# Performance work log

Hardware: AMD Instinct MI355X
Metric: run time of the kernel (lower is better)

The kernel has to match this reference:

```python
import jax, jax.numpy as jnp
import numpy as np

# Sizes: N nodes, E edges, C channels (atoms/node), CF channel_nf, R relations,
# H hidden/feature dim (uniform across the 2 AM_EGCL layers), L layers.
N, E, C, CF, R, H, L = 10000, 160000, 4, 16, 7, 256, 2
EPS = 1e-5


def setup_inputs() -> dict:
    key = jax.random.key(0)
    ks = jax.random.split(key, 16)
    p = lambda k, shape: (jax.random.normal(k, shape, jnp.float32) * 0.02)
    inp = {
        "input": jax.random.normal(ks[0], (N, H), jnp.float32),
        "coords": jax.random.normal(ks[1], (N, C, 3), jnp.float32),
        "channel_attr": jax.random.normal(ks[2], (N, C, CF), jnp.float32),
        # strictly positive channel weights (atom-occupancy style)
        "channel_weights": jax.random.uniform(ks[3], (N, C), jnp.float32) + 0.5,
        "edge_weights": jax.random.uniform(ks[4], (E,), jnp.float32),
    }
    src = jax.random.randint(ks[5], (E,), 0, N)
    dst = jax.random.randint(ks[6], (E,), 0, N)
    rel = jax.random.randint(ks[7], (E,), 0, R)
    inp["edge_list"] = jnp.stack([src, dst, rel], axis=1)
    ein = 2 * H + CF + 2 * CF  # h_i, h_j, radial feat, pooled channel attr i/j
    inp.update({
        "W_rad": p(ks[8], (L, C * C, CF)), "b_rad": jnp.zeros((L, CF), jnp.float32),
        "W_e1": p(ks[9], (L, ein, H)), "b_e1": jnp.zeros((L, H), jnp.float32),
        "W_e2": p(ks[10], (L, H, H)), "b_e2": jnp.zeros((L, H), jnp.float32),
        "W_c1": p(ks[11], (L, H, H)), "b_c1": jnp.zeros((L, H), jnp.float32),
        "W_c2": p(ks[12], (L, H, C * C)),
        "W_n1": p(ks[13], (L, R * H + H, H)), "b_n1": jnp.zeros((L, H), jnp.float32),
        "W_n2": p(ks[14], (L, H, H)), "b_n2": jnp.zeros((L, H), jnp.float32),
        "ln_g": jnp.ones((L, H), jnp.float32), "ln_b": jnp.zeros((L, H), jnp.float32),
    })
    return inp


def _am_egcl(h, x, edge_list, channel_attr, channel_weights, edge_weights, prm):
    """One adaptive multichannel equivariant graph conv layer."""
    (W_rad, b_rad, W_e1, b_e1, W_e2, b_e2, W_c1, b_c1, W_c2,
     W_n1, b_n1, W_n2, b_n2, ln_g, ln_b) = prm
    row, col, rel = edge_list[:, 0], edge_list[:, 1], edge_list[:, 2]
    # --- multichannel invariant radial features -------------------------------
    xd = x[row][:, :, None, :] - x[col][:, None, :, :]        # [E,C,C,3]
    radial = jnp.sum(xd * xd, axis=-1)                         # [E,C,C]
    wmask = channel_weights[row][:, :, None] * channel_weights[col][:, None, :]
    radial = radial * wmask
    rad_feat = jax.nn.silu(radial.reshape(-1, C * C) @ W_rad + b_rad)  # [E,CF]
    # pooled (weighted-mean) channel attribute per node
    csum = jnp.sum(channel_weights, axis=-1, keepdims=True)
    ca = jnp.sum(channel_attr * channel_weights[..., None], axis=1) / csum  # [N,CF]
    # --- edge message MLP ------------------------------------------------------
    m_in = jnp.concatenate([h[row], h[col], rad_feat, ca[row], ca[col]], axis=-1)
    m = jax.nn.silu(jax.nn.silu(m_in @ W_e1 + b_e1) @ W_e2 + b_e2)  # [E,H]
    m = m * edge_weights[:, None]
    # --- equivariant coord update ---------------------------------------------
    phi = (jax.nn.silu(m @ W_c1 + b_c1) @ W_c2).reshape(-1, C, C)   # [E,C,C]
    trans = jnp.mean(xd * phi[..., None], axis=2)                   # [E,C,3]
    ones = jnp.ones((trans.shape[0],), x.dtype)
    cnt = jnp.maximum(jax.ops.segment_sum(ones, row, num_segments=N), 1.0)
    x_out = x + jax.ops.segment_sum(trans, row, num_segments=N) / cnt[:, None, None]
    # --- relational node aggregation (GearNet-style, per-relation bins) --------
    seg = col * R + rel
    agg = jax.ops.segment_sum(m, seg, num_segments=N * R).reshape(N, R * H)
    h_out = jax.nn.silu(jnp.concatenate([agg, h], axis=-1) @ W_n1 + b_n1) @ W_n2 + b_n2
    # dropout p=0 (eval) -> identity; then LayerNorm
    mu = jnp.mean(h_out, axis=-1, keepdims=True)
    var = jnp.var(h_out, axis=-1, keepdims=True)
    h_out = (h_out - mu) * jax.lax.rsqrt(var + EPS) * ln_g + ln_b
    return h_out, x_out


def reference(input, edge_list, coords, channel_attr, channel_weights, edge_weights,
              W_rad, b_rad, W_e1, b_e1, W_e2, b_e2, W_c1, b_c1, W_c2,
              W_n1, b_n1, W_n2, b_n2, ln_g, ln_b):
    h, x = input, coords
    for i in range(L):  # fixed small layer count
        prm = (W_rad[i], b_rad[i], W_e1[i], b_e1[i], W_e2[i], b_e2[i],
               W_c1[i], b_c1[i], W_c2[i], W_n1[i], b_n1[i], W_n2[i], b_n2[i],
               ln_g[i], ln_b[i])
        h, x = _am_egcl(h, x, edge_list, channel_attr, channel_weights,
                        edge_weights, prm)
    return h, x  # (node_feature [N,H], coord_feature [N,C,3])
```

## Files before the change

### kernel.cpp

```cpp
#include <hip/hip_runtime.h>
#include <hip/hip_bf16.h>

#define NN 10000
#define EE 160000
#define CCH 4
#define CF 16
#define RR 7
#define HH 256
#define NSEG 70000
#define SCB 274
#define EPSV 1e-5f

typedef unsigned short ushort_t;
typedef __bf16 bf16x8 __attribute__((ext_vector_type(8)));
typedef float f32x4 __attribute__((ext_vector_type(4)));

__device__ __forceinline__ float silu_f(float v) {
    float e = __builtin_amdgcn_exp2f(v * -1.442695040888963f);
    return v * __builtin_amdgcn_rcpf(1.f + e);
}

__device__ __forceinline__ ushort_t bf16u(float f) {
    unsigned int u = __builtin_bit_cast(unsigned int, f);
    u += 0x7fffu + ((u >> 16) & 1u);
    return (ushort_t)(u >> 16);
}

__device__ __forceinline__ float ubf2f(ushort_t u) {
    unsigned int v = ((unsigned int)u) << 16;
    return __builtin_bit_cast(float, v);
}


__global__ __launch_bounds__(256) void cab_kernel(
    const float* __restrict__ attr, const float* __restrict__ cw,
    ushort_t* __restrict__ cab16)
{
    int t = blockIdx.x * 256 + threadIdx.x;
    if (t < NN * CF) {
        int n = t >> 4, f = t & 15;
        float s = 0.f, cs = 0.f;
        #pragma unroll
        for (int c = 0; c < CCH; ++c) {
            float w = cw[n * CCH + c];
            s  += attr[(n * CCH + c) * CF + f] * w;
            cs += w;
        }
        cab16[t] = bf16u(s / cs);
    }
}

__global__ __launch_bounds__(256) void cvt_kernel(
    const float* __restrict__ s, ushort_t* __restrict__ d, int n)
{
    int t = blockIdx.x * 256 + threadIdx.x;
    if (t < n) d[t] = bf16u(s[t]);
}

__global__ __launch_bounds__(256) void histdeg_kernel(
    const int* __restrict__ el, int* __restrict__ hist, float* __restrict__ deg)
{
    int e = blockIdx.x * 256 + threadIdx.x;
    if (e < EE) {
        int r = el[e * 3], c = el[e * 3 + 1], rl = el[e * 3 + 2];
        atomicAdd(&hist[c * RR + rl], 1);
        atomicAdd(&deg[r], 1.f);
    }
}

__global__ __launch_bounds__(256) void scan1_kernel(
    const int* __restrict__ hist, int* __restrict__ pscan, int* __restrict__ bsum)
{
    __shared__ int sc[256];
    int b = blockIdx.x, t = threadIdx.x, i = b * 256 + t;
    int v = (i < NSEG) ? hist[i] : 0;
    sc[t] = v; __syncthreads();
    for (int off = 1; off < 256; off <<= 1) {
        int u = (t >= off) ? sc[t - off] : 0;
        __syncthreads();
        sc[t] += u;
        __syncthreads();
    }
    if (i < NSEG) pscan[i] = sc[t] - v;
    if (t == 255) bsum[b] = sc[255];
}

__global__ __launch_bounds__(256) void scan2_kernel(
    const int* __restrict__ bsum, int* __restrict__ bofs, int nb)
{
    __shared__ int sc[512];
    int t = threadIdx.x;
    int o1 = (t < nb) ? bsum[t] : 0;
    int o2 = (t + 256 < nb) ? bsum[t + 256] : 0;
    sc[t] = o1; sc[t + 256] = o2;
    __syncthreads();
    for (int off = 1; off < 512; off <<= 1) {
        int u1 = (t >= off) ? sc[t - off] : 0;
        int u2 = (t + 256 >= off) ? sc[t + 256 - off] : 0;
        __syncthreads();
        sc[t] += u1; sc[t + 256] += u2;
        __syncthreads();
    }
    if (t < nb) bofs[t] = sc[t] - o1;
    if (t + 256 < nb) bofs[t + 256] = sc[t + 256] - o2;
}

__global__ __launch_bounds__(256) void scan3_kernel(
    const int* __restrict__ pscan, const int* __restrict__ bofs, int* __restrict__ segst)
{
    int b = blockIdx.x, t = threadIdx.x, i = b * 256 + t;
    if (i < NSEG) segst[i] = pscan[i] + bofs[b];
    if (i == 0) segst[NSEG] = EE;
}

__global__ __launch_bounds__(256) void scatter_kernel(
    const int* __restrict__ el, const int* __restrict__ segst,
    int* __restrict__ cursor, int* __restrict__ perm)
{
    int e = blockIdx.x * 256 + threadIdx.x;
    if (e < EE) {
        int s = el[e * 3 + 1] * RR + el[e * 3 + 2];
        int pos = segst[s] + atomicAdd(&cursor[s], 1);
        perm[pos] = e;
    }
}


__device__ __forceinline__ void pack_tile(
    const float* __restrict__ W, ushort_t* __restrict__ out,
    int Kreal, int N, int kt, int nt, int NTOT, int lane)
{
    int n = nt * 16 + (lane & 15);
    int kbase = kt * 32 + (lane >> 4) * 8;
    ushort_t* o = out + ((size_t)(kt * NTOT + nt) * 64 + lane) * 8;
    #pragma unroll
    for (int j = 0; j < 8; ++j) {
        int k = kbase + j;
        o[j] = (k < Kreal) ? bf16u(W[(size_t)k * N + n]) : (ushort_t)0;
    }
}

__global__ __launch_bounds__(64) void pack_all_kernel(
    const float* __restrict__ W_e1, const float* __restrict__ W_e2,
    const float* __restrict__ W_c1, const float* __restrict__ W_c2,
    const float* __restrict__ W_n1, const float* __restrict__ W_n2,
    ushort_t* __restrict__ pe1, ushort_t* __restrict__ pe2,
    ushort_t* __restrict__ pc1, ushort_t* __restrict__ pc2,
    ushort_t* __restrict__ pn1, ushort_t* __restrict__ pn2)
{
    int b = blockIdx.x, lane = threadIdx.x;
    int l = 0;
    if (b >= 1704) { l = 1; b -= 1704; }
    if (b < 288) {
        pack_tile(W_e1 + (size_t)l * 143360, pe1 + (size_t)l * 147456,
                  560, 256, b / 16, b & 15, 16, lane);
    } else if (b < 416) {
        int c = b - 288;
        pack_tile(W_e2 + (size_t)l * 65536, pe2 + (size_t)l * 65536,
                  256, 256, c / 16, c & 15, 16, lane);
    } else if (b < 544) {
        int c = b - 416;
        pack_tile(W_c1 + (size_t)l * 65536, pc1 + (size_t)l * 65536,
                  256, 256, c / 16, c & 15, 16, lane);
    } else if (b < 552) {
        int c = b - 544;
        pack_tile(W_c2 + (size_t)l * 4096, pc2 + (size_t)l * 4096,
                  256, 16, c, 0, 1, lane);
    } else if (b < 1576) {
        int c = b - 552;
        pack_tile(W_n1 + (size_t)l * 524288, pn1 + (size_t)l * 524288,
                  2048, 256, c / 16, c & 15, 16, lane);
    } else {
        int c = b - 1576;
        pack_tile(W_n2 + (size_t)l * 65536, pn2 + (size_t)l * 65536,
                  256, 256, c / 16, c & 15, 16, lane);
    }
}


template<int KT, int NTOT>
__device__ __forceinline__ void mfma_stage32(
    const ushort_t (&A)[32][584], int colOff,
    const ushort_t* __restrict__ Wp, int w, int lane,
    f32x4 (&acc)[2][4])
{
    const f32x4 Z = {0.f, 0.f, 0.f, 0.f};
    #pragma unroll
    for (int mt = 0; mt < 2; ++mt)
        #pragma unroll
        for (int j = 0; j < 4; ++j) acc[mt][j] = Z;
    const int ar = lane & 15, aq = (lane >> 4) * 8;
    for (int kt = 0; kt < KT; ++kt) {
        bf16x8 a0 = *(const bf16x8*)&A[ar][colOff + kt * 32 + aq];
        bf16x8 a1 = *(const bf16x8*)&A[16 + ar][colOff + kt * 32 + aq];
        #pragma unroll
        for (int j = 0; j < 4; ++j) {
            bf16x8 b = *(const bf16x8*)(Wp + ((size_t)(kt * NTOT + w * 4 + j) * 64 + lane) * 8);
            acc[0][j] = __builtin_amdgcn_mfma_f32_16x16x32_bf16(a0, b, acc[0][j], 0, 0, 0);
            acc[1][j] = __builtin_amdgcn_mfma_f32_16x16x32_bf16(a1, b, acc[1][j], 0, 0, 0);
        }
    }
}


__global__ __launch_bounds__(256, 4) void edge_kernel(
    const int* __restrict__ el, const int* __restrict__ perm,
    const float* __restrict__ cw,
    const float* __restrict__ ew, const float* __restrict__ x,
    const ushort_t* __restrict__ hb16, const ushort_t* __restrict__ cab16,
    const float* __restrict__ W_rad, const float* __restrict__ b_rad,
    const ushort_t* __restrict__ pe1, const float* __restrict__ b_e1,
    const ushort_t* __restrict__ pe2, const float* __restrict__ b_e2,
    const ushort_t* __restrict__ pc1, const float* __restrict__ b_c1,
    const ushort_t* __restrict__ pc2,
    ushort_t* __restrict__ mb16, float* __restrict__ xacc)
{
    __shared__ ushort_t abuf[32][584];
    __shared__ float radbuf[32][16];
    __shared__ int rowS[32], colS[32];
    __shared__ float ewS[32];

    const int tid = threadIdx.x, lane = tid & 63, w = tid >> 6;
    const int ar = lane & 15, aq = (lane >> 4) * 8, quad = lane >> 4;
    const int e0 = blockIdx.x * 32;

    if (tid < 32) {
        int eg = perm[e0 + tid];
        rowS[tid] = el[eg * 3 + 0];
        colS[tid] = el[eg * 3 + 1];
        ewS[tid]  = ew[eg];
    }
    __syncthreads();

    #pragma unroll
    for (int it = 0; it < 8; ++it) {
        int c = it * 256 + tid;
        int e = c >> 6, half = (c >> 5) & 1, idx = c & 31;
        int node = half ? colS[e] : rowS[e];
        *(uint4*)&abuf[e][half * 256 + idx * 8] =
            ((const uint4*)(hb16 + (size_t)node * 256))[idx];
    }
    if (tid < 128) {
        int e = tid >> 2, half2 = (tid >> 1) & 1, idx = tid & 1;
        int node = half2 ? colS[e] : rowS[e];
        *(uint4*)&abuf[e][528 + half2 * 16 + idx * 8] =
            ((const uint4*)(cab16 + node * 16))[idx];
    } else if (tid < 192) {
        int c = tid - 128, e = c >> 1, idx = c & 1;
        uint4 z = {0u, 0u, 0u, 0u};
        *(uint4*)&abuf[e][560 + idx * 8] = z;
    }
    #pragma unroll
    for (int it = 0; it < 2; ++it) {
        int t = it * 256 + tid;
        int e = t >> 4, ab = t & 15, a = ab >> 2, b = ab & 3;
        int row = rowS[e], col = colS[e];
        float d0 = x[row * 12 + a * 3 + 0] - x[col * 12 + b * 3 + 0];
        float d1 = x[row * 12 + a * 3 + 1] - x[col * 12 + b * 3 + 1];
        float d2 = x[row * 12 + a * 3 + 2] - x[col * 12 + b * 3 + 2];
        radbuf[e][ab] = (d0 * d0 + d1 * d1 + d2 * d2)
                      * cw[row * CCH + a] * cw[col * CCH + b];
    }
    __syncthreads();

    #pragma unroll
    for (int it = 0; it < 2; ++it) {
        int t = it * 256 + tid;
        int e = t >> 4, f = t & 15;
        float acc = b_rad[f];
        #pragma unroll
        for (int ab = 0; ab < 16; ++ab) acc += radbuf[e][ab] * W_rad[ab * 16 + f];
        abuf[e][512 + f] = bf16u(silu_f(acc));
    }
    __syncthreads();

    f32x4 acc[2][4];

    mfma_stage32<18, 16>(abuf, 0, pe1, w, lane, acc);
    __syncthreads();
    #pragma unroll
    for (int j = 0; j < 4; ++j) {
        int n = w * 64 + j * 16 + ar;
        float bj = b_e1[n];
        #pragma unroll
        for (int mt = 0; mt < 2; ++mt)
            #pragma unroll
            for (int r = 0; r < 4; ++r)
                abuf[mt * 16 + quad * 4 + r][288 + n] = bf16u(silu_f(acc[mt][j][r] + bj));
    }
    __syncthreads();

    mfma_stage32<8, 16>(abuf, 288, pe2, w, lane, acc);
    #pragma unroll
    for (int j = 0; j < 4; ++j) {
        int n = w * 64 + j * 16 + ar;
        float bj = b_e2[n];
        #pragma unroll
        for (int mt = 0; mt < 2; ++mt)
            #pragma unroll
            for (int r = 0; r < 4; ++r) {
                int e = mt * 16 + quad * 4 + r;
                abuf[e][n] = bf16u(silu_f(acc[mt][j][r] + bj) * ewS[e]);
            }
    }
    __syncthreads();

    #pragma unroll
    for (int it = 0; it < 4; ++it) {
        int t = it * 256 + tid;
        int e = t >> 5, c = t & 31;
        *(uint4*)(mb16 + ((size_t)(e0 + e) * 256 + c * 8)) =
            *(const uint4*)&abuf[e][c * 8];
    }

    mfma_stage32<8, 16>(abuf, 0, pc1, w, lane, acc);
    #pragma unroll
    for (int j = 0; j < 4; ++j) {
        int n = w * 64 + j * 16 + ar;
        float bj = b_c1[n];
        #pragma unroll
        for (int mt = 0; mt < 2; ++mt)
            #pragma unroll
            for (int r = 0; r < 4; ++r)
                abuf[mt * 16 + quad * 4 + r][288 + n] = bf16u(silu_f(acc[mt][j][r] + bj));
    }
    __syncthreads();

    if (w < 2) {
        const f32x4 Z = {0.f, 0.f, 0.f, 0.f};
        f32x4 p = Z;
        #pragma unroll
        for (int kt = 0; kt < 8; ++kt) {
            bf16x8 a = *(const bf16x8*)&abuf[w * 16 + ar][288 + kt * 32 + aq];
            bf16x8 b = *(const bf16x8*)(pc2 + ((size_t)kt * 64 + lane) * 8);
            p = __builtin_amdgcn_mfma_f32_16x16x32_bf16(a, b, p, 0, 0, 0);
        }
        #pragma unroll
        for (int r = 0; r < 4; ++r)
            radbuf[w * 16 + quad * 4 + r][ar] = p[r];
    }
    __syncthreads();

    for (int t = tid; t < 384; t += 256) {
        int e = t / 12, r = t - e * 12, a = r / 3, k = r - a * 3;
        int row = rowS[e], col = colS[e];
        float xr = x[row * 12 + a * 3 + k];
        float s = 0.f;
        #pragma unroll
        for (int b = 0; b < 4; ++b)
            s += (xr - x[col * 12 + b * 3 + k]) * radbuf[e][a * 4 + b];
        atomicAdd(&xacc[row * 12 + a * 3 + k], 0.25f * s);
    }
}


__global__ __launch_bounds__(256, 3) void node_kernel(
    const ushort_t* __restrict__ mb16, const int* __restrict__ segst,
    const ushort_t* __restrict__ pn1, const float* __restrict__ b_n1,
    const ushort_t* __restrict__ pn2, const float* __restrict__ b_n2,
    const float* __restrict__ ln_g, const float* __restrict__ ln_b,
    float* __restrict__ h_out, ushort_t* __restrict__ hb16)
{
    __shared__ __align__(16) char arena[33024];
    __shared__ ushort_t tbuf[16][264];
    __shared__ float redS[16][16], red2S[16][16], muS[16], rsS[16];
    ushort_t (*nbuf)[1032] = (ushort_t(*)[1032])arena;
    float (*h2buf)[264] = (float(*)[264])arena;

    const int tid = threadIdx.x, lane = tid & 63, w = tid >> 6;
    const int n0 = blockIdx.x * 16;
    const int ar = lane & 15, aq = (lane >> 4) * 8;
    const f32x4 Z = {0.f, 0.f, 0.f, 0.f};

    f32x4 acc[4] = {Z, Z, Z, Z};
    for (int chunk = 0; chunk < 2; ++chunk) {
        for (int ln = 0; ln < 4; ++ln) {
            int node = w * 4 + ln;
            int gnode = n0 + node;
            if (chunk == 0) {
                #pragma unroll
                for (int r = 0; r < 4; ++r) {
                    int s = gnode * RR + r;
                    int beg = segst[s], end = segst[s + 1];
                    float a0 = 0.f, a1 = 0.f, a2 = 0.f, a3 = 0.f;
                    for (int e = beg; e < end; ++e) {
                        ushort4 u = *(const ushort4*)(mb16 + (size_t)e * 256 + lane * 4);
                        a0 += ubf2f(u.x); a1 += ubf2f(u.y);
                        a2 += ubf2f(u.z); a3 += ubf2f(u.w);
                    }
                    ushort4 o;
                    o.x = bf16u(a0); o.y = bf16u(a1); o.z = bf16u(a2); o.w = bf16u(a3);
                    *(ushort4*)&nbuf[node][r * 256 + lane * 4] = o;
                }
            } else {
                #pragma unroll
                for (int r = 4; r < 7; ++r) {
                    int s = gnode * RR + r;
                    int beg = segst[s], end = segst[s + 1];
                    float a0 = 0.f, a1 = 0.f, a2 = 0.f, a3 = 0.f;
                    for (int e = beg; e < end; ++e) {
                        ushort4 u = *(const ushort4*)(mb16 + (size_t)e * 256 + lane * 4);
                        a0 += ubf2f(u.x); a1 += ubf2f(u.y);
                        a2 += ubf2f(u.z); a3 += ubf2f(u.w);
                    }
                    ushort4 o;
                    o.x = bf16u(a0); o.y = bf16u(a1); o.z = bf16u(a2); o.w = bf16u(a3);
                    *(ushort4*)&nbuf[node][(r - 4) * 256 + lane * 4] = o;
                }
                *(ushort4*)&nbuf[node][768 + lane * 4] =
                    *(const ushort4*)(hb16 + (size_t)gnode * 256 + lane * 4);
            }
        }
        __syncthreads();
        for (int kt = 0; kt < 32; ++kt) {
            bf16x8 a = *(const bf16x8*)&nbuf[ar][kt * 32 + aq];
            int ktg = chunk * 32 + kt;
            #pragma unroll
            for (int j = 0; j < 4; ++j) {
                bf16x8 b = *(const bf16x8*)(pn1 + ((size_t)(ktg * 16 + w * 4 + j) * 64 + lane) * 8);
                acc[j] = __builtin_amdgcn_mfma_f32_16x16x32_bf16(a, b, acc[j], 0, 0, 0);
            }
        }
        __syncthreads();
    }
    #pragma unroll
    for (int j = 0; j < 4; ++j) {
        int n = w * 64 + j * 16 + ar;
        float bj = b_n1[n];
        #pragma unroll
        for (int r = 0; r < 4; ++r)
            tbuf[(lane >> 4) * 4 + r][n] = bf16u(silu_f(acc[j][r] + bj));
    }
    __syncthreads();
    f32x4 acc2[4] = {Z, Z, Z, Z};
    for (int kt = 0; kt < 8; ++kt) {
        bf16x8 a = *(const bf16x8*)&tbuf[ar][kt * 32 + aq];
        #pragma unroll
        for (int j = 0; j < 4; ++j) {
            bf16x8 b = *(const bf16x8*)(pn2 + ((size_t)(kt * 16 + w * 4 + j) * 64 + lane) * 8);
            acc2[j] = __builtin_amdgcn_mfma_f32_16x16x32_bf16(a, b, acc2[j], 0, 0, 0);
        }
    }
    float hv[4][4];
    #pragma unroll
    for (int j = 0; j < 4; ++j) {
        int n = w * 64 + j * 16 + ar;
        float bj = b_n2[n];
        #pragma unroll
        for (int r = 0; r < 4; ++r) {
            hv[j][r] = acc2[j][r] + bj;
            h2buf[(lane >> 4) * 4 + r][n] = hv[j][r];
        }
    }
    __syncthreads();
    {
        int node = tid >> 4, c = tid & 15;
        float s = 0.f, s2 = 0.f;
        #pragma unroll
        for (int i = 0; i < 16; ++i) {
            float v = h2buf[node][c * 16 + i];
            s += v; s2 += v * v;
        }
        redS[node][c] = s; red2S[node][c] = s2;
    }
    __syncthreads();
    if (tid < 16) {
        float s = 0.f, s2 = 0.f;
        #pragma unroll
        for (int c = 0; c < 16; ++c) { s += redS[tid][c]; s2 += red2S[tid][c]; }
        float mu = s * (1.f / 256.f);
        muS[tid] = mu;
        rsS[tid] = rsqrtf(s2 * (1.f / 256.f) - mu * mu + EPSV);
    }
    __syncthreads();
    #pragma unroll
    for (int j = 0; j < 4; ++j) {
        int n = w * 64 + j * 16 + ar;
        float g = ln_g[n], bb = ln_b[n];
        #pragma unroll
        for (int r = 0; r < 4; ++r) {
            int row = (lane >> 4) * 4 + r;
            float v = (hv[j][r] - muS[row]) * rsS[row] * g + bb;
            h_out[(size_t)(n0 + row) * HH + n] = v;
            hb16[(size_t)(n0 + row) * HH + n] = bf16u(v);
        }
    }
}

__global__ __launch_bounds__(256) void xout_kernel(
    const float* __restrict__ x_in, const float* __restrict__ xacc,
    const float* __restrict__ deg, float* __restrict__ x_out)
{
    int t = blockIdx.x * 256 + threadIdx.x;
    if (t < NN * 12) {
        int n = t / 12;
        float c = fmaxf(deg[n], 1.f);
        x_out[t] = x_in[t] + xacc[t] / c;
    }
}


extern "C" void kernel_launch(void* const* d_in, const int* in_sizes, int n_in,
                              void* d_out, int out_size, void* d_ws, size_t ws_size,
                              hipStream_t stream)
{
    const float* input  = (const float*)d_in[0];
    const float* coords = (const float*)d_in[1];
    const float* cattr  = (const float*)d_in[2];
    const float* cwts   = (const float*)d_in[3];
    const float* ewts   = (const float*)d_in[4];
    const int*   elist  = (const int*)d_in[5];
    const float* W_rad  = (const float*)d_in[6];
    const float* b_rad  = (const float*)d_in[7];
    const float* W_e1   = (const float*)d_in[8];
    const float* b_e1   = (const float*)d_in[9];
    const float* W_e2   = (const float*)d_in[10];
    const float* b_e2   = (const float*)d_in[11];
    const float* W_c1   = (const float*)d_in[12];
    const float* b_c1   = (const float*)d_in[13];
    const float* W_c2   = (const float*)d_in[14];
    const float* W_n1   = (const float*)d_in[15];
    const float* b_n1   = (const float*)d_in[16];
    const float* W_n2   = (const float*)d_in[17];
    const float* b_n2   = (const float*)d_in[18];
    const float* ln_g   = (const float*)d_in[19];
    const float* ln_b   = (const float*)d_in[20];

    float* wsf  = (float*)d_ws;
    float* deg  = wsf;
    float* xacc = deg + 10000;
    float* xbuf = xacc + 120000;
    int* ip     = (int*)(xbuf + 120000);
    int* hist   = ip;
    int* pscan  = hist + 70000;
    int* cursor = pscan + 70000;
    int* segst  = cursor + 70000;
    int* bsum   = segst + 70001;
    int* bofs   = bsum + 512;
    int* perm   = bofs + 512;
    ushort_t* up = (ushort_t*)(((uintptr_t)(perm + 160000) + 15) & ~(uintptr_t)15);
    ushort_t* hb16  = up;
    ushort_t* cab16 = hb16 + 2560000;
    ushort_t* mb16  = cab16 + 160000;
    ushort_t* pe1   = mb16 + 40960000;
    ushort_t* pe2   = pe1 + 294912;
    ushort_t* pc1   = pe2 + 131072;
    ushort_t* pc2   = pc1 + 131072;
    ushort_t* pn1   = pc2 + 8192;
    ushort_t* pn2   = pn1 + 1048576;

    hipMemsetAsync(deg, 0, (size_t)NN * sizeof(float), stream);
    hipMemsetAsync(hist, 0, (size_t)NSEG * sizeof(int), stream);
    hipMemsetAsync(cursor, 0, (size_t)NSEG * sizeof(int), stream);

    cab_kernel<<<(NN * CF + 255) / 256, 256, 0, stream>>>(cattr, cwts, cab16);
    cvt_kernel<<<(NN * HH + 255) / 256, 256, 0, stream>>>(input, hb16, NN * HH);
    histdeg_kernel<<<(EE + 255) / 256, 256, 0, stream>>>(elist, hist, deg);

    scan1_kernel<<<SCB, 256, 0, stream>>>(hist, pscan, bsum);
    scan2_kernel<<<1, 256, 0, stream>>>(bsum, bofs, SCB);
    scan3_kernel<<<SCB, 256, 0, stream>>>(pscan, bofs, segst);
    scatter_kernel<<<(EE + 255) / 256, 256, 0, stream>>>(elist, segst, cursor, perm);

    pack_all_kernel<<<3408, 64, 0, stream>>>(
        W_e1, W_e2, W_c1, W_c2, W_n1, W_n2,
        pe1, pe2, pc1, pc2, pn1, pn2);

    for (int l = 0; l < 2; ++l) {
        const float* x_in = (l == 0) ? coords : xbuf;
        float* h_out = (float*)d_out;
        float* x_out = (l == 0) ? xbuf : ((float*)d_out + (size_t)NN * HH);

        hipMemsetAsync(xacc, 0, (size_t)NN * 12 * sizeof(float), stream);

        edge_kernel<<<EE / 32, 256, 0, stream>>>(
            elist, perm, cwts, ewts, x_in, hb16, cab16,
            W_rad + l * 256, b_rad + l * 16,
            pe1 + (size_t)l * 147456, b_e1 + l * HH,
            pe2 + (size_t)l * 65536,  b_e2 + l * HH,
            pc1 + (size_t)l * 65536,  b_c1 + l * HH,
            pc2 + (size_t)l * 4096,
            mb16, xacc);

        node_kernel<<<NN / 16, 256, 0, stream>>>(
            mb16, segst,
            pn1 + (size_t)l * 524288, b_n1 + l * HH,
            pn2 + (size_t)l * 65536,  b_n2 + l * HH,
            ln_g + l * HH, ln_b + l * HH,
            h_out, hb16);

        xout_kernel<<<(NN * 12 + 255) / 256, 256, 0, stream>>>(
            x_in, xacc, deg, x_out);
    }
}
```

Baseline: 600.7 us.

## Precompute per-node halves of first edge MLP layer before edge gather

The first edge-MLP matmul is linear in the concatenated [h_i, h_j, radial, ca_i, ca_j] input, so the node-dependent parts are now computed once per node by a new kernel into A (row side, with bias) and B (col side). Each edge then gathers A[row]+B[col] and only does a small K=32 MFMA for the radial features. This replaces a K=576 matmul per edge (160k edges) with a K=288 matmul per node (10k nodes). The cost is an extra kernel launch, extra bf16 intermediate buffers, and additional bf16 rounding of the partial sums before the silu.

```diff
diff --git a/kernel.cpp b/kernel.cpp
--- a/kernel.cpp
+++ b/kernel.cpp
@@ -140,40 +140,153 @@
     }
 }
 
+__device__ __forceinline__ void pack_ab_tile(
+    const float* __restrict__ W_e1, ushort_t* __restrict__ pab,
+    int kt, int nt, int lane)
+{
+    int nl = nt * 16 + (lane & 15);
+    int kbase = kt * 32 + (lane >> 4) * 8;
+    ushort_t* o = pab + ((size_t)(kt * 32 + nt) * 64 + lane) * 8;
+    #pragma unroll
+    for (int j = 0; j < 8; ++j) {
+        int k = kbase + j;
+        float v = 0.f;
+        if (k < 256) {
+            v = (nl < 256) ? W_e1[(size_t)k * 256 + nl]
+                           : W_e1[(size_t)(256 + k) * 256 + (nl - 256)];
+        } else if (k < 272) {
+            int kk = k - 256;
+            v = (nl < 256) ? W_e1[(size_t)(528 + kk) * 256 + nl]
+                           : W_e1[(size_t)(544 + kk) * 256 + (nl - 256)];
+        }
+        o[j] = bf16u(v);
+    }
+}
+
+__device__ __forceinline__ void pack_e1c_tile(
+    const float* __restrict__ W_e1, ushort_t* __restrict__ pe1c,
+    int nt, int lane)
+{
+    int n = nt * 16 + (lane & 15);
+    int kbase = (lane >> 4) * 8;
+    ushort_t* o = pe1c + ((size_t)nt * 64 + lane) * 8;
+    #pragma unroll
+    for (int j = 0; j < 8; ++j) {
+        int k = kbase + j;
+        o[j] = (k < 16) ? bf16u(W_e1[(size_t)(512 + k) * 256 + n]) : (ushort_t)0;
+    }
+}
+
 __global__ __launch_bounds__(64) void pack_all_kernel(
     const float* __restrict__ W_e1, const float* __restrict__ W_e2,
     const float* __restrict__ W_c1, const float* __restrict__ W_c2,
     const float* __restrict__ W_n1, const float* __restrict__ W_n2,
-    ushort_t* __restrict__ pe1, ushort_t* __restrict__ pe2,
+    ushort_t* __restrict__ pab, ushort_t* __restrict__ pe1c,
+    ushort_t* __restrict__ pe2,
     ushort_t* __restrict__ pc1, ushort_t* __restrict__ pc2,
     ushort_t* __restrict__ pn1, ushort_t* __restrict__ pn2)
 {
     int b = blockIdx.x, lane = threadIdx.x;
     int l = 0;
-    if (b >= 1704) { l = 1; b -= 1704; }
+    if (b >= 1720) { l = 1; b -= 1720; }
+    const float* We1 = W_e1 + (size_t)l * 143360;
     if (b < 288) {
-        pack_tile(W_e1 + (size_t)l * 143360, pe1 + (size_t)l * 147456,
-                  560, 256, b / 16, b & 15, 16, lane);
-    } else if (b < 416) {
-        int c = b - 288;
+        pack_ab_tile(We1, pab + (size_t)l * 147456, b / 32, b % 32, lane);
+    } else if (b < 304) {
+        pack_e1c_tile(We1, pe1c + (size_t)l * 8192, b - 288, lane);
+    } else if (b < 432) {
+        int c = b - 304;
         pack_tile(W_e2 + (size_t)l * 65536, pe2 + (size_t)l * 65536,
                   256, 256, c / 16, c & 15, 16, lane);
-    } else if (b < 544) {
-        int c = b - 416;
+    } else if (b < 560) {
+        int c = b - 432;
         pack_tile(W_c1 + (size_t)l * 65536, pc1 + (size_t)l * 65536,
                   256, 256, c / 16, c & 15, 16, lane);
-    } else if (b < 552) {
-        int c = b - 544;
+    } else if (b < 568) {
+        int c = b - 560;
         pack_tile(W_c2 + (size_t)l * 4096, pc2 + (size_t)l * 4096,
                   256, 16, c, 0, 1, lane);
-    } else if (b < 1576) {
-        int c = b - 552;
+    } else if (b < 1592) {
+        int c = b - 568;
         pack_tile(W_n1 + (size_t)l * 524288, pn1 + (size_t)l * 524288,
                   2048, 256, c / 16, c & 15, 16, lane);
     } else {
-        int c = b - 1576;
+        int c = b - 1592;
         pack_tile(W_n2 + (size_t)l * 65536, pn2 + (size_t)l * 65536,
                   256, 256, c / 16, c & 15, 16, lane);
+    }
+}
+
+
+__global__ __launch_bounds__(256, 3) void abk_kernel(
+    const ushort_t* __restrict__ hb16, const ushort_t* __restrict__ cab16,
+    const ushort_t* __restrict__ pab, const float* __restrict__ b_e1,
+    ushort_t* __restrict__ A16, ushort_t* __restrict__ B16)
+{
+    __shared__ ushort_t inbuf[32][296];
+    __shared__ ushort_t obuf[32][520];
+    const int tid = threadIdx.x, lane = tid & 63, w = tid >> 6;
+    const int ar = lane & 15, aq = (lane >> 4) * 8, quad = lane >> 4;
+    const int n0 = blockIdx.x * 32;
+    const uint4 z4 = {0u, 0u, 0u, 0u};
+
+    #pragma unroll
+    for (int it = 0; it < 4; ++it) {
+        int c = it * 256 + tid;
+        int e = c >> 5, i4 = c & 31;
+        int node = n0 + e;
+        uint4 v = (node < NN) ? ((const uint4*)(hb16 + (size_t)node * 256))[i4] : z4;
+        *(uint4*)&inbuf[e][i4 * 8] = v;
+    }
+    if (tid < 64) {
+        int e = tid >> 1, i4 = tid & 1;
+        int node = n0 + e;
+        uint4 v = (node < NN) ? ((const uint4*)(cab16 + node * 16))[i4] : z4;
+        *(uint4*)&inbuf[e][256 + i4 * 8] = v;
+    } else if (tid < 128) {
+        int c = tid - 64, e = c >> 1, i4 = c & 1;
+        *(uint4*)&inbuf[e][272 + i4 * 8] = z4;
+    }
+    __syncthreads();
+
+    const f32x4 Z = {0.f, 0.f, 0.f, 0.f};
+    f32x4 acc[2][8];
+    #pragma unroll
+    for (int mt = 0; mt < 2; ++mt)
+        #pragma unroll
+        for (int jt = 0; jt < 8; ++jt) acc[mt][jt] = Z;
+    for (int kt = 0; kt < 9; ++kt) {
+        bf16x8 a0 = *(const bf16x8*)&inbuf[ar][kt * 32 + aq];
+        bf16x8 a1 = *(const bf16x8*)&inbuf[16 + ar][kt * 32 + aq];
+        #pragma unroll
+        for (int jt = 0; jt < 8; ++jt) {
+            bf16x8 b = *(const bf16x8*)(pab + ((size_t)(kt * 32 + w * 8 + jt) * 64 + lane) * 8);
+            acc[0][jt] = __builtin_amdgcn_mfma_f32_16x16x32_bf16(a0, b, acc[0][jt], 0, 0, 0);
+            acc[1][jt] = __builtin_amdgcn_mfma_f32_16x16x32_bf16(a1, b, acc[1][jt], 0, 0, 0);
+        }
+    }
+    #pragma unroll
+    for (int jt = 0; jt < 8; ++jt) {
+        int n = w * 128 + jt * 16 + ar;
+        float bias = (n < 256) ? b_e1[n] : 0.f;
+        #pragma unroll
+        for (int mt = 0; mt < 2; ++mt)
+            #pragma unroll
+            for (int r = 0; r < 4; ++r)
+                obuf[mt * 16 + quad * 4 + r][n] = bf16u(acc[mt][jt][r] + bias);
+    }
+    __syncthreads();
+    #pragma unroll
+    for (int it = 0; it < 8; ++it) {
+        int c = it * 256 + tid;
+        int e = c >> 6, i4 = c & 63;
+        int node = n0 + e;
+        if (node < NN) {
+            if (i4 < 32)
+                *(uint4*)(A16 + (size_t)node * 256 + i4 * 8) = *(const uint4*)&obuf[e][i4 * 8];
+            else
+                *(uint4*)(B16 + (size_t)node * 256 + (i4 - 32) * 8) = *(const uint4*)&obuf[e][256 + (i4 - 32) * 8];
+        }
     }
 }
 
@@ -207,9 +320,9 @@
     const int* __restrict__ el, const int* __restrict__ perm,
     const float* __restrict__ cw,
     const float* __restrict__ ew, const float* __restrict__ x,
-    const ushort_t* __restrict__ hb16, const ushort_t* __restrict__ cab16,
+    const ushort_t* __restrict__ A16, const ushort_t* __restrict__ B16,
     const float* __restrict__ W_rad, const float* __restrict__ b_rad,
-    const ushort_t* __restrict__ pe1, const float* __restrict__ b_e1,
+    const ushort_t* __restrict__ pe1c,
     const ushort_t* __restrict__ pe2, const float* __restrict__ b_e2,
     const ushort_t* __restrict__ pc1, const float* __restrict__ b_c1,
     const ushort_t* __restrict__ pc2,
@@ -233,22 +346,16 @@
     __syncthreads();
 
     #pragma unroll
-    for (int it = 0; it < 8; ++it) {
+    for (int it = 0; it < 4; ++it) {
         int c = it * 256 + tid;
-        int e = c >> 6, half = (c >> 5) & 1, idx = c & 31;
-        int node = half ? colS[e] : rowS[e];
-        *(uint4*)&abuf[e][half * 256 + idx * 8] =
-            ((const uint4*)(hb16 + (size_t)node * 256))[idx];
-    }
-    if (tid < 128) {
-        int e = tid >> 2, half2 = (tid >> 1) & 1, idx = tid & 1;
-        int node = half2 ? colS[e] : rowS[e];
-        *(uint4*)&abuf[e][528 + half2 * 16 + idx * 8] =
-            ((const uint4*)(cab16 + node * 16))[idx];
-    } else if (tid < 192) {
-        int c = tid - 128, e = c >> 1, idx = c & 1;
-        uint4 z = {0u, 0u, 0u, 0u};
-        *(uint4*)&abuf[e][560 + idx * 8] = z;
+        int e = c >> 5, i4 = c & 31;
+        bf16x8 va = *(const bf16x8*)((const uint4*)(A16 + (size_t)rowS[e] * 256) + i4);
+        bf16x8 vb = *(const bf16x8*)((const uint4*)(B16 + (size_t)colS[e] * 256) + i4);
+        bf16x8 vs;
+        #pragma unroll
+        for (int j = 0; j < 8; ++j)
+            vs[j] = (__bf16)((float)va[j] + (float)vb[j]);
+        *(bf16x8*)&abuf[e][288 + i4 * 8] = vs;
     }
     #pragma unroll
     for (int it = 0; it < 2; ++it) {
@@ -270,23 +377,25 @@
         float acc = b_rad[f];
         #pragma unroll
         for (int ab = 0; ab < 16; ++ab) acc += radbuf[e][ab] * W_rad[ab * 16 + f];
-        abuf[e][512 + f] = bf16u(silu_f(acc));
+        abuf[e][f] = bf16u(silu_f(acc));
+        abuf[e][16 + f] = 0;
     }
     __syncthreads();
 
     f32x4 acc[2][4];
 
-    mfma_stage32<18, 16>(abuf, 0, pe1, w, lane, acc);
-    __syncthreads();
+    mfma_stage32<1, 16>(abuf, 0, pe1c, w, lane, acc);
     #pragma unroll
     for (int j = 0; j < 4; ++j) {
         int n = w * 64 + j * 16 + ar;
-        float bj = b_e1[n];
         #pragma unroll
         for (int mt = 0; mt < 2; ++mt)
             #pragma unroll
-            for (int r = 0; r < 4; ++r)
-                abuf[mt * 16 + quad * 4 + r][288 + n] = bf16u(silu_f(acc[mt][j][r] + bj));
+            for (int r = 0; r < 4; ++r) {
+                int e = mt * 16 + quad * 4 + r;
+                float s = ubf2f(abuf[e][288 + n]) + acc[mt][j][r];
+                abuf[e][288 + n] = bf16u(silu_f(s));
+            }
     }
     __syncthreads();
 
@@ -542,8 +651,11 @@
     ushort_t* hb16  = up;
     ushort_t* cab16 = hb16 + 2560000;
     ushort_t* mb16  = cab16 + 160000;
-    ushort_t* pe1   = mb16 + 40960000;
-    ushort_t* pe2   = pe1 + 294912;
+    ushort_t* A16   = mb16 + 40960000;
+    ushort_t* B16   = A16 + 2560000;
+    ushort_t* pab   = B16 + 2560000;
+    ushort_t* pe1c  = pab + 294912;
+    ushort_t* pe2   = pe1c + 16384;
     ushort_t* pc1   = pe2 + 131072;
     ushort_t* pc2   = pc1 + 131072;
     ushort_t* pn1   = pc2 + 8192;
@@ -562,9 +674,9 @@
     scan3_kernel<<<SCB, 256, 0, stream>>>(pscan, bofs, segst);
     scatter_kernel<<<(EE + 255) / 256, 256, 0, stream>>>(elist, segst, cursor, perm);
 
-    pack_all_kernel<<<3408, 64, 0, stream>>>(
+    pack_all_kernel<<<3440, 64, 0, stream>>>(
         W_e1, W_e2, W_c1, W_c2, W_n1, W_n2,
-        pe1, pe2, pc1, pc2, pn1, pn2);
+        pab, pe1c, pe2, pc1, pc2, pn1, pn2);
 
     for (int l = 0; l < 2; ++l) {
         const float* x_in = (l == 0) ? coords : xbuf;
@@ -573,10 +685,13 @@
 
         hipMemsetAsync(xacc, 0, (size_t)NN * 12 * sizeof(float), stream);
 
+        abk_kernel<<<(NN + 31) / 32, 256, 0, stream>>>(
+            hb16, cab16, pab + (size_t)l * 147456, b_e1 + l * HH, A16, B16);
+
         edge_kernel<<<EE / 32, 256, 0, stream>>>(
-            elist, perm, cwts, ewts, x_in, hb16, cab16,
+            elist, perm, cwts, ewts, x_in, A16, B16,
             W_rad + l * 256, b_rad + l * 16,
-            pe1 + (size_t)l * 147456, b_e1 + l * HH,
+            pe1c + (size_t)l * 8192,
             pe2 + (size_t)l * 65536,  b_e2 + l * HH,
             pc1 + (size_t)l * 65536,  b_c1 + l * HH,
             pc2 + (size_t)l * 4096,
```

Measured after the change: 524.7 us. 1.14x faster.
